# Kernel tuning notes

Measured on AMD Instinct MI355X. Metric: run time of the kernel, lower is better.

## Reference

```python
import jax, jax.numpy as jnp
import numpy as np

D_MODEL, N_HEADS = 768, 12
D_K = D_MODEL // N_HEADS
NEG = -1e9


def setup_inputs() -> dict:
    key = jax.random.key(0)
    ks = jax.random.split(key, 12)
    B, S, D = 2, 4096, D_MODEL
    s = 1.0 / np.sqrt(D)
    inp = {
        'query': jax.random.normal(ks[0], (B, S, D), jnp.float32),
        'key': jax.random.normal(ks[1], (B, S, D), jnp.float32),
        'value': jax.random.normal(ks[2], (B, S, D), jnp.float32),
        'mask': jnp.ones((B, S), jnp.int32),
        'Wq': jax.random.normal(ks[3], (D, D), jnp.float32) * s,
        'bq': jnp.zeros((D,), jnp.float32),
        'Wk': jax.random.normal(ks[4], (D, D), jnp.float32) * s,
        'bk': jnp.zeros((D,), jnp.float32),
        'Wv': jax.random.normal(ks[5], (D, D), jnp.float32) * s,
        'bv': jnp.zeros((D,), jnp.float32),
        'Wo': jax.random.normal(ks[6], (D, D), jnp.float32) * s,
        'bo': jnp.zeros((D,), jnp.float32),
    }
    return inp


def reference(query, key, value, mask, Wq, bq, Wk, bk, Wv, bv, Wo, bo):
    B, Sq, D = query.shape
    Sk = key.shape[1]
    # torch Linear: x @ W.T + b; weights stored [out, in]
    def proj(x, W, b, S):
        return (x @ W.T + b).reshape(B, S, N_HEADS, D_K).transpose(0, 2, 1, 3)
    Q = proj(query, Wq, bq, Sq)   # [B,H,Sq,Dk]
    K = proj(key, Wk, bk, Sk)
    V = proj(value, Wv, bv, Sk)
    scores = jnp.einsum('bhqd,bhkd->bhqk', Q, K) / jnp.sqrt(jnp.float32(D_K))
    # padding mask on keys: [B,1,1,Sk]
    scores = jnp.where(mask[:, None, None, :] == 0, NEG, scores)
    # causal mask (triu, diagonal=1)
    causal = jnp.triu(jnp.ones((Sq, Sk), bool), k=1)
    scores = jnp.where(causal[None, None], NEG, scores)
    attn = jax.nn.softmax(scores, axis=-1)
    out = jnp.einsum('bhqk,bhkd->bhqd', attn, V)
    out = out.transpose(0, 2, 1, 3).reshape(B, Sq, D)
    return out @ Wo.T + bo
```

## Files before the change

kernel.cpp:

```cpp
#include <hip/hip_runtime.h>
#include <hip/hip_bf16.h>

#define D_MODEL 768
#define N_HEADS 12
#define D_K     64
#define NEG_INF (-1e9f)
#define KS_PAD  72
#define VT_PAD  136
#define SCALE_Q 0.1803368801111154f
#define W_ELEMS (D_MODEL * D_MODEL)

typedef __attribute__((ext_vector_type(8))) short          bf16x8;
typedef __attribute__((ext_vector_type(4))) float          floatx4;
typedef __attribute__((ext_vector_type(4))) unsigned short ushortx4;
typedef __attribute__((ext_vector_type(2))) unsigned int   uintx2;
typedef __attribute__((ext_vector_type(4))) unsigned int   uintx4;

static __device__ __forceinline__ unsigned short f2bf(float f) {
    unsigned u = __builtin_bit_cast(unsigned, f);
    u += 0x7FFFu + ((u >> 16) & 1u);
    return (unsigned short)(u >> 16);
}

static __device__ __forceinline__ void gload_lds16(const void* g, void* l) {
    __builtin_amdgcn_global_load_lds(
        (const __attribute__((address_space(1))) void*)g,
        (__attribute__((address_space(3))) void*)l, 16, 0, 0);
}

__global__ __launch_bounds__(256) void convert_w4(
    const float* __restrict__ W0, const float* __restrict__ W1,
    const float* __restrict__ W2, const float* __restrict__ W3,
    unsigned short* __restrict__ out)
{
    const float* src[4] = {W0, W1, W2, W3};
    const float* W = src[blockIdx.y];
    unsigned short* o = out + (size_t)blockIdx.y * W_ELEMS;
    const int i = (blockIdx.x * 256 + threadIdx.x) * 4;
    float4 v = *(const float4*)(W + i);
    ushortx4 h = { f2bf(v.x), f2bf(v.y), f2bf(v.z), f2bf(v.w) };
    *(ushortx4*)(o + i) = h;
}

__global__ __launch_bounds__(256) void convert_a3(
    const float* __restrict__ A0, const float* __restrict__ A1,
    const float* __restrict__ A2,
    unsigned short* __restrict__ O0, unsigned short* __restrict__ O1,
    unsigned short* __restrict__ O2)
{
    const int z = blockIdx.y;
    const float* A = (z == 0) ? A0 : (z == 1) ? A1 : A2;
    unsigned short* O = (z == 0) ? O0 : (z == 1) ? O1 : O2;
    const int i = (blockIdx.x * 256 + threadIdx.x) * 4;
    float4 v = *(const float4*)(A + i);
    ushortx4 h = { f2bf(v.x), f2bf(v.y), f2bf(v.z), f2bf(v.w) };
    *(ushortx4*)(O + i) = h;
}

template <bool QKV>
__global__ __launch_bounds__(256) void gemm128(
    const unsigned short* __restrict__ A0, const unsigned short* __restrict__ A1,
    const unsigned short* __restrict__ A2,
    const unsigned short* __restrict__ W0, const unsigned short* __restrict__ W1,
    const unsigned short* __restrict__ W2,
    const float* __restrict__ b0, const float* __restrict__ b1,
    const float* __restrict__ b2,
    void* __restrict__ C0, void* __restrict__ C1, void* __restrict__ C2,
    int S)
{
    __shared__ __align__(16) unsigned short As[128 * 32];
    __shared__ __align__(16) unsigned short Bs[128 * 32];

    const int z = QKV ? blockIdx.z : 0;
    const unsigned short* A = (z == 0) ? A0 : (z == 1) ? A1 : A2;
    const unsigned short* W = (z == 0) ? W0 : (z == 1) ? W1 : W2;
    const float* bias       = (z == 0) ? b0 : (z == 1) ? b1 : b2;
    void* C                 = (z == 0) ? C0 : (z == 1) ? C1 : C2;
    const float scale = (QKV && z == 0) ? SCALE_Q : 1.0f;
    const int mode = QKV ? ((z == 2) ? 3 : 1) : 0;

    const int tid  = threadIdx.x;
    const int wave = tid >> 6;
    const int lane = tid & 63;
    const int quad = lane >> 4;
    const int l16  = lane & 15;
    const int m0 = blockIdx.x * 128;
    const int n0 = blockIdx.y * 128;
    const int wm = (wave & 1) * 64;
    const int wn = (wave >> 1) * 64;
    const int sr = lane >> 2;
    const int sc = (lane & 3) << 3;

    const floatx4 zero4 = {0.f, 0.f, 0.f, 0.f};
    floatx4 acc[4][4];
    #pragma unroll
    for (int i = 0; i < 4; ++i)
        #pragma unroll
        for (int j = 0; j < 4; ++j) acc[i][j] = zero4;

    for (int k0 = 0; k0 < D_MODEL; k0 += 32) {
        #pragma unroll
        for (int c = 0; c < 2; ++c) {
            const int row = wave * 32 + c * 16;
            gload_lds16(A + (size_t)(m0 + row + sr) * D_MODEL + k0 + sc,
                        As + row * 32);
            gload_lds16(W + (size_t)(n0 + row + sr) * D_MODEL + k0 + sc,
                        Bs + row * 32);
        }
        __syncthreads();

        bf16x8 af[4], bfr[4];
        #pragma unroll
        for (int i = 0; i < 4; ++i)
            af[i] = *(const bf16x8*)(As + (wm + i * 16 + l16) * 32 + quad * 8);
        #pragma unroll
        for (int j = 0; j < 4; ++j)
            bfr[j] = *(const bf16x8*)(Bs + (wn + j * 16 + l16) * 32 + quad * 8);
        #pragma unroll
        for (int i = 0; i < 4; ++i)
            #pragma unroll
            for (int j = 0; j < 4; ++j)
                acc[i][j] = __builtin_amdgcn_mfma_f32_16x16x32_bf16(
                    bfr[j], af[i], acc[i][j], 0, 0, 0);
        __syncthreads();
    }

    #pragma unroll
    for (int i = 0; i < 4; ++i) {
        const int m = m0 + wm + i * 16 + l16;
        #pragma unroll
        for (int j = 0; j < 4; ++j) {
            const int nb = n0 + wn + j * 16 + quad * 4;
            const float4 bv = *(const float4*)(bias + nb);
            float v0 = (acc[i][j][0] + bv.x) * scale;
            float v1 = (acc[i][j][1] + bv.y) * scale;
            float v2 = (acc[i][j][2] + bv.z) * scale;
            float v3 = (acc[i][j][3] + bv.w) * scale;
            if (mode == 0) {
                float4 o = {v0, v1, v2, v3};
                *(float4*)((float*)C + (size_t)m * D_MODEL + nb) = o;
            } else if (mode == 1) {
                ushortx4 o = {f2bf(v0), f2bf(v1), f2bf(v2), f2bf(v3)};
                *(ushortx4*)((unsigned short*)C + (size_t)m * D_MODEL + nb) = o;
            } else {
                const int bb = m / S, s = m - bb * S;
                const int hh = nb >> 6, d = nb & 63;
                unsigned short* base = (unsigned short*)C +
                    ((size_t)(bb * N_HEADS + hh) * D_K + d) * S + s;
                base[0]         = f2bf(v0);
                base[(size_t)S]     = f2bf(v1);
                base[(size_t)S * 2] = f2bf(v2);
                base[(size_t)S * 3] = f2bf(v3);
            }
        }
    }
}

__global__ __launch_bounds__(256) void flash_attn(
    const unsigned short* __restrict__ Qp,
    const unsigned short* __restrict__ Kp,
    const unsigned short* __restrict__ VpT,
    const int* __restrict__ mask,
    unsigned short* __restrict__ O,
    int S)
{
    __shared__ __align__(16) unsigned short Ks [128 * KS_PAD];
    __shared__ __align__(16) unsigned short Vts[64 * VT_PAD];
    __shared__ __align__(16) float mskf[128];

    const int L  = blockIdx.x;
    const int bh = L % 24;
    const int p  = L / 24;
    const int h  = bh % 12;
    const int b  = bh / 12;
    const int nqt = S >> 6;
    const int tid  = threadIdx.x;
    const int wave = tid >> 6;
    const int lane = tid & 63;
    const int quad = lane >> 4;
    const int l16  = lane & 15;

    const unsigned short* Kbase = Kp  + (size_t)(b * S) * D_MODEL + h * D_K;
    const unsigned short* Vbase = VpT + (size_t)(b * N_HEADS + h) * D_K * S;

    const floatx4 zero4 = {0.f, 0.f, 0.f, 0.f};
    const short one_bf = (short)0x3F80;
    const bf16x8 ones = {one_bf, one_bf, one_bf, one_bf,
                         one_bf, one_bf, one_bf, one_bf};

    #pragma unroll
    for (int sel = 0; sel < 2; ++sel) {
        const int qt = sel ? (nqt - 1 - p) : p;
        const int q0 = qt * 64;
        const int qbase = q0 + wave * 16;
        const int qabs = qbase + l16;

        const size_t rowQ = (size_t)(b * S + qbase + l16) * D_MODEL + h * D_K;
        const bf16x8 qf0 = *(const bf16x8*)(Qp + rowQ + quad * 8);
        const bf16x8 qf1 = *(const bf16x8*)(Qp + rowQ + 32 + quad * 8);

        floatx4 acc2[4];
        floatx4 acc_l = zero4;
        #pragma unroll
        for (int dt = 0; dt < 4; ++dt) acc2[dt] = zero4;

        const int ni = (qt >> 1) + 1;
        for (int kt = 0; kt < ni; ++kt) {
            const int k0 = kt * 128;
            #pragma unroll
            for (int g = tid; g < 1024; g += 256) {
                const int krow = g >> 3, kc = (g & 7) << 3;
                *(bf16x8*)(Ks + krow * KS_PAD + kc) =
                    *(const bf16x8*)(Kbase + (size_t)(k0 + krow) * D_MODEL + kc);
                const int vrow = g >> 4, vc = (g & 15) << 3;
                *(bf16x8*)(Vts + vrow * VT_PAD + vc) =
                    *(const bf16x8*)(Vbase + (size_t)vrow * S + k0 + vc);
            }
            if (tid < 128)
                mskf[tid] = (mask[b * S + k0 + tid] == 0) ? NEG_INF : 0.f;
            __syncthreads();

            floatx4 s[8];
            #pragma unroll
            for (int nt = 0; nt < 8; ++nt) {
                floatx4 c = *(const floatx4*)(mskf + nt * 16 + quad * 4);
                bf16x8 kf0 = *(const bf16x8*)(Ks + (nt * 16 + l16) * KS_PAD + quad * 8);
                bf16x8 kf1 = *(const bf16x8*)(Ks + (nt * 16 + l16) * KS_PAD + 32 + quad * 8);
                c = __builtin_amdgcn_mfma_f32_16x16x32_bf16(kf0, qf0, c, 0, 0, 0);
                c = __builtin_amdgcn_mfma_f32_16x16x32_bf16(kf1, qf1, c, 0, 0, 0);
                s[nt] = c;
            }

            if (kt == ni - 1) {
                #pragma unroll
                for (int nt = 0; nt < 8; ++nt) {
                    const int kb = k0 + nt * 16 + quad * 4;
                    #pragma unroll
                    for (int r = 0; r < 4; ++r)
                        if (kb + r > qabs) s[nt][r] = NEG_INF;
                }
            }

            unsigned pk0[8], pk1[8];
            #pragma unroll
            for (int nt = 0; nt < 8; ++nt) {
                const float e0 = __builtin_exp2f(s[nt][0]);
                const float e1 = __builtin_exp2f(s[nt][1]);
                const float e2 = __builtin_exp2f(s[nt][2]);
                const float e3 = __builtin_exp2f(s[nt][3]);
                pk0[nt] = __builtin_amdgcn_perm(__builtin_bit_cast(unsigned, e1),
                                                __builtin_bit_cast(unsigned, e0), 0x07060302u);
                pk1[nt] = __builtin_amdgcn_perm(__builtin_bit_cast(unsigned, e3),
                                                __builtin_bit_cast(unsigned, e2), 0x07060302u);
            }

            #pragma unroll
            for (int kh = 0; kh < 4; ++kh) {
                uintx2 a32 = __builtin_amdgcn_permlane32_swap(
                    pk0[2 * kh], pk0[2 * kh + 1], false, false);
                uintx2 b32 = __builtin_amdgcn_permlane32_swap(
                    pk1[2 * kh], pk1[2 * kh + 1], false, false);
                uintx2 a16 = __builtin_amdgcn_permlane16_swap(
                    a32[0], a32[1], false, false);
                uintx2 b16 = __builtin_amdgcn_permlane16_swap(
                    b32[0], b32[1], false, false);
                const uintx4 pw = {a16[0], b16[0], a16[1], b16[1]};
                const bf16x8 pf = __builtin_bit_cast(bf16x8, pw);
                #pragma unroll
                for (int dt = 0; dt < 4; ++dt) {
                    bf16x8 vf = *(const bf16x8*)(Vts + (dt * 16 + l16) * VT_PAD + kh * 32 + quad * 8);
                    acc2[dt] = __builtin_amdgcn_mfma_f32_16x16x32_bf16(pf, vf, acc2[dt], 0, 0, 0);
                }
                acc_l = __builtin_amdgcn_mfma_f32_16x16x32_bf16(pf, ones, acc_l, 0, 0, 0);
            }
            __syncthreads();
        }

        #pragma unroll
        for (int r = 0; r < 4; ++r) {
            const float inv = 1.f / acc_l[r];
            const int gq = qbase + quad * 4 + r;
            const size_t base = (size_t)(b * S + gq) * D_MODEL + h * D_K;
            #pragma unroll
            for (int dt = 0; dt < 4; ++dt)
                O[base + dt * 16 + l16] = f2bf(acc2[dt][r] * inv);
        }
        __syncthreads();
    }
}

extern "C" void kernel_launch(void* const* d_in, const int* in_sizes, int n_in,
                              void* d_out, int out_size, void* d_ws, size_t ws_size,
                              hipStream_t stream) {
    const float* query = (const float*)d_in[0];
    const float* key   = (const float*)d_in[1];
    const float* value = (const float*)d_in[2];
    const int*   mask  = (const int*)d_in[3];
    const float* Wq = (const float*)d_in[4];
    const float* bq = (const float*)d_in[5];
    const float* Wk = (const float*)d_in[6];
    const float* bk = (const float*)d_in[7];
    const float* Wv = (const float*)d_in[8];
    const float* bv = (const float*)d_in[9];
    const float* Wo = (const float*)d_in[10];
    const float* bo = (const float*)d_in[11];

    const int B  = 2;
    const int BS = in_sizes[3];
    const int S  = BS / B;
    const int M  = BS;

    unsigned short* Qp  = (unsigned short*)d_ws;
    unsigned short* Kp  = Qp  + (size_t)M * D_MODEL;
    unsigned short* VpT = Kp  + (size_t)M * D_MODEL;
    unsigned short* Obf = VpT + (size_t)M * D_MODEL;
    unsigned short* Wbf = Obf + (size_t)M * D_MODEL;
    unsigned short* Wqb = Wbf;
    unsigned short* Wkb = Wbf + (size_t)W_ELEMS;
    unsigned short* Wvb = Wbf + (size_t)W_ELEMS * 2;
    unsigned short* Wob = Wbf + (size_t)W_ELEMS * 3;
    unsigned short* ka = (unsigned short*)d_out;
    unsigned short* va = ka + (size_t)M * D_MODEL;

    dim3 blk(256);
    convert_w4<<<dim3(W_ELEMS / 1024, 4), blk, 0, stream>>>(Wq, Wk, Wv, Wo, Wbf);
    convert_a3<<<dim3((M * D_MODEL) / 1024, 3), blk, 0, stream>>>(
        query, key, value, Obf, ka, va);

    gemm128<true><<<dim3(M / 128, D_MODEL / 128, 3), blk, 0, stream>>>(
        Obf, ka, va, Wqb, Wkb, Wvb, bq, bk, bv, Qp, Kp, VpT, S);

    flash_attn<<<768, blk, 0, stream>>>(Qp, Kp, VpT, mask, Obf, S);

    gemm128<false><<<dim3(M / 128, D_MODEL / 128, 1), blk, 0, stream>>>(
        Obf, Obf, Obf, Wob, Wob, Wob, bo, bo, bo,
        d_out, d_out, d_out, S);
}
```

Baseline: 314.3 us.

## One query tile per block, heaviest-first, with XOR-swizzled unpadded LDS and direct mask loads

The attention kernel now assigns a single 64-row query tile to each block, launched heaviest-first (descending qt), instead of pairing a light and a heavy tile per block across 768 blocks. The grid doubles to 24*(S/64) blocks. LDS padding is replaced by an XOR swizzle on K and V^T rows, which reduces shared memory per block. Mask values are now read straight from global memory into the score accumulator init rather than staged in LDS, and __launch_bounds__ adds a 5-blocks-per-CU occupancy hint. Together these aim to improve load balance and occupancy, at the cost of more blocks and repeated global mask reads.

```diff
diff --git a/kernel.cpp b/kernel.cpp
--- a/kernel.cpp
+++ b/kernel.cpp
@@ -5,8 +5,6 @@
 #define N_HEADS 12
 #define D_K     64
 #define NEG_INF (-1e9f)
-#define KS_PAD  72
-#define VT_PAD  136
 #define SCALE_Q 0.1803368801111154f
 #define W_ELEMS (D_MODEL * D_MODEL)
 
@@ -156,7 +154,7 @@
     }
 }
 
-__global__ __launch_bounds__(256) void flash_attn(
+__global__ __launch_bounds__(256, 5) void flash_attn(
     const unsigned short* __restrict__ Qp,
     const unsigned short* __restrict__ Kp,
     const unsigned short* __restrict__ VpT,
@@ -164,128 +162,131 @@
     unsigned short* __restrict__ O,
     int S)
 {
-    __shared__ __align__(16) unsigned short Ks [128 * KS_PAD];
-    __shared__ __align__(16) unsigned short Vts[64 * VT_PAD];
-    __shared__ __align__(16) float mskf[128];
-
-    const int L  = blockIdx.x;
-    const int bh = L % 24;
-    const int p  = L / 24;
-    const int h  = bh % 12;
-    const int b  = bh / 12;
+    __shared__ __align__(16) unsigned short Ks [128 * 64];
+    __shared__ __align__(16) unsigned short Vts[64 * 128];
+
+    const int L   = blockIdx.x;
+    const int bh  = L % 24;
+    const int idx = L / 24;
+    const int h   = bh % 12;
+    const int b   = bh / 12;
     const int nqt = S >> 6;
+    const int qt  = nqt - 1 - idx;
     const int tid  = threadIdx.x;
     const int wave = tid >> 6;
     const int lane = tid & 63;
     const int quad = lane >> 4;
     const int l16  = lane & 15;
+    const int kxor = (l16 & 7) << 3;
 
     const unsigned short* Kbase = Kp  + (size_t)(b * S) * D_MODEL + h * D_K;
     const unsigned short* Vbase = VpT + (size_t)(b * N_HEADS + h) * D_K * S;
+    const int* mbase = mask + b * S;
 
     const floatx4 zero4 = {0.f, 0.f, 0.f, 0.f};
     const short one_bf = (short)0x3F80;
     const bf16x8 ones = {one_bf, one_bf, one_bf, one_bf,
                          one_bf, one_bf, one_bf, one_bf};
 
+    const int q0 = qt * 64;
+    const int qbase = q0 + wave * 16;
+    const int qabs = qbase + l16;
+
+    const size_t rowQ = (size_t)(b * S + qbase + l16) * D_MODEL + h * D_K;
+    const bf16x8 qf0 = *(const bf16x8*)(Qp + rowQ + quad * 8);
+    const bf16x8 qf1 = *(const bf16x8*)(Qp + rowQ + 32 + quad * 8);
+
+    floatx4 acc2[4];
+    floatx4 acc_l = zero4;
     #pragma unroll
-    for (int sel = 0; sel < 2; ++sel) {
-        const int qt = sel ? (nqt - 1 - p) : p;
-        const int q0 = qt * 64;
-        const int qbase = q0 + wave * 16;
-        const int qabs = qbase + l16;
-
-        const size_t rowQ = (size_t)(b * S + qbase + l16) * D_MODEL + h * D_K;
-        const bf16x8 qf0 = *(const bf16x8*)(Qp + rowQ + quad * 8);
-        const bf16x8 qf1 = *(const bf16x8*)(Qp + rowQ + 32 + quad * 8);
-
-        floatx4 acc2[4];
-        floatx4 acc_l = zero4;
-        #pragma unroll
-        for (int dt = 0; dt < 4; ++dt) acc2[dt] = zero4;
-
-        const int ni = (qt >> 1) + 1;
-        for (int kt = 0; kt < ni; ++kt) {
-            const int k0 = kt * 128;
-            #pragma unroll
-            for (int g = tid; g < 1024; g += 256) {
-                const int krow = g >> 3, kc = (g & 7) << 3;
-                *(bf16x8*)(Ks + krow * KS_PAD + kc) =
-                    *(const bf16x8*)(Kbase + (size_t)(k0 + krow) * D_MODEL + kc);
-                const int vrow = g >> 4, vc = (g & 15) << 3;
-                *(bf16x8*)(Vts + vrow * VT_PAD + vc) =
-                    *(const bf16x8*)(Vbase + (size_t)vrow * S + k0 + vc);
-            }
-            if (tid < 128)
-                mskf[tid] = (mask[b * S + k0 + tid] == 0) ? NEG_INF : 0.f;
-            __syncthreads();
-
-            floatx4 s[8];
+    for (int dt = 0; dt < 4; ++dt) acc2[dt] = zero4;
+
+    const int ni = (qt >> 1) + 1;
+    for (int kt = 0; kt < ni; ++kt) {
+        const int k0 = kt * 128;
+        #pragma unroll
+        for (int g = tid; g < 1024; g += 256) {
+            const int krow = g >> 3, kc = (g & 7) << 3;
+            *(bf16x8*)(Ks + krow * 64 + (kc ^ ((krow & 7) << 3))) =
+                *(const bf16x8*)(Kbase + (size_t)(k0 + krow) * D_MODEL + kc);
+            const int vrow = g >> 4, vc = (g & 15) << 3;
+            *(bf16x8*)(Vts + vrow * 128 + (vc ^ ((vrow & 7) << 3))) =
+                *(const bf16x8*)(Vbase + (size_t)vrow * S + k0 + vc);
+        }
+        __syncthreads();
+
+        floatx4 s[8];
+        #pragma unroll
+        for (int nt = 0; nt < 8; ++nt) {
+            const int4 mk = *(const int4*)(mbase + k0 + nt * 16 + quad * 4);
+            floatx4 c;
+            c[0] = (mk.x == 0) ? NEG_INF : 0.f;
+            c[1] = (mk.y == 0) ? NEG_INF : 0.f;
+            c[2] = (mk.z == 0) ? NEG_INF : 0.f;
+            c[3] = (mk.w == 0) ? NEG_INF : 0.f;
+            const int krow = nt * 16 + l16;
+            bf16x8 kf0 = *(const bf16x8*)(Ks + krow * 64 + ((quad * 8) ^ kxor));
+            bf16x8 kf1 = *(const bf16x8*)(Ks + krow * 64 + ((32 + quad * 8) ^ kxor));
+            c = __builtin_amdgcn_mfma_f32_16x16x32_bf16(kf0, qf0, c, 0, 0, 0);
+            c = __builtin_amdgcn_mfma_f32_16x16x32_bf16(kf1, qf1, c, 0, 0, 0);
+            s[nt] = c;
+        }
+
+        if (kt == ni - 1) {
             #pragma unroll
             for (int nt = 0; nt < 8; ++nt) {
-                floatx4 c = *(const floatx4*)(mskf + nt * 16 + quad * 4);
-                bf16x8 kf0 = *(const bf16x8*)(Ks + (nt * 16 + l16) * KS_PAD + quad * 8);
-                bf16x8 kf1 = *(const bf16x8*)(Ks + (nt * 16 + l16) * KS_PAD + 32 + quad * 8);
-                c = __builtin_amdgcn_mfma_f32_16x16x32_bf16(kf0, qf0, c, 0, 0, 0);
-                c = __builtin_amdgcn_mfma_f32_16x16x32_bf16(kf1, qf1, c, 0, 0, 0);
-                s[nt] = c;
+                const int kb = k0 + nt * 16 + quad * 4;
+                #pragma unroll
+                for (int r = 0; r < 4; ++r)
+                    if (kb + r > qabs) s[nt][r] = NEG_INF;
             }
-
-            if (kt == ni - 1) {
-                #pragma unroll
-                for (int nt = 0; nt < 8; ++nt) {
-                    const int kb = k0 + nt * 16 + quad * 4;
-                    #pragma unroll
-                    for (int r = 0; r < 4; ++r)
-                        if (kb + r > qabs) s[nt][r] = NEG_INF;
-                }
+        }
+
+        unsigned pk0[8], pk1[8];
+        #pragma unroll
+        for (int nt = 0; nt < 8; ++nt) {
+            const float e0 = __builtin_exp2f(s[nt][0]);
+            const float e1 = __builtin_exp2f(s[nt][1]);
+            const float e2 = __builtin_exp2f(s[nt][2]);
+            const float e3 = __builtin_exp2f(s[nt][3]);
+            pk0[nt] = __builtin_amdgcn_perm(__builtin_bit_cast(unsigned, e1),
+                                            __builtin_bit_cast(unsigned, e0), 0x07060302u);
+            pk1[nt] = __builtin_amdgcn_perm(__builtin_bit_cast(unsigned, e3),
+                                            __builtin_bit_cast(unsigned, e2), 0x07060302u);
+        }
+
+        #pragma unroll
+        for (int kh = 0; kh < 4; ++kh) {
+            uintx2 a32 = __builtin_amdgcn_permlane32_swap(
+                pk0[2 * kh], pk0[2 * kh + 1], false, false);
+            uintx2 b32 = __builtin_amdgcn_permlane32_swap(
+                pk1[2 * kh], pk1[2 * kh + 1], false, false);
+            uintx2 a16 = __builtin_amdgcn_permlane16_swap(
+                a32[0], a32[1], false, false);
+            uintx2 b16 = __builtin_amdgcn_permlane16_swap(
+                b32[0], b32[1], false, false);
+            const uintx4 pw = {a16[0], b16[0], a16[1], b16[1]};
+            const bf16x8 pf = __builtin_bit_cast(bf16x8, pw);
+            #pragma unroll
+            for (int dt = 0; dt < 4; ++dt) {
+                const int vrow = dt * 16 + l16;
+                bf16x8 vf = *(const bf16x8*)(
+                    Vts + vrow * 128 + ((kh * 32 + quad * 8) ^ kxor));
+                acc2[dt] = __builtin_amdgcn_mfma_f32_16x16x32_bf16(pf, vf, acc2[dt], 0, 0, 0);
             }
-
-            unsigned pk0[8], pk1[8];
-            #pragma unroll
-            for (int nt = 0; nt < 8; ++nt) {
-                const float e0 = __builtin_exp2f(s[nt][0]);
-                const float e1 = __builtin_exp2f(s[nt][1]);
-                const float e2 = __builtin_exp2f(s[nt][2]);
-                const float e3 = __builtin_exp2f(s[nt][3]);
-                pk0[nt] = __builtin_amdgcn_perm(__builtin_bit_cast(unsigned, e1),
-                                                __builtin_bit_cast(unsigned, e0), 0x07060302u);
-                pk1[nt] = __builtin_amdgcn_perm(__builtin_bit_cast(unsigned, e3),
-                                                __builtin_bit_cast(unsigned, e2), 0x07060302u);
-            }
-
-            #pragma unroll
-            for (int kh = 0; kh < 4; ++kh) {
-                uintx2 a32 = __builtin_amdgcn_permlane32_swap(
-                    pk0[2 * kh], pk0[2 * kh + 1], false, false);
-                uintx2 b32 = __builtin_amdgcn_permlane32_swap(
-                    pk1[2 * kh], pk1[2 * kh + 1], false, false);
-                uintx2 a16 = __builtin_amdgcn_permlane16_swap(
-                    a32[0], a32[1], false, false);
-                uintx2 b16 = __builtin_amdgcn_permlane16_swap(
-                    b32[0], b32[1], false, false);
-                const uintx4 pw = {a16[0], b16[0], a16[1], b16[1]};
-                const bf16x8 pf = __builtin_bit_cast(bf16x8, pw);
-                #pragma unroll
-                for (int dt = 0; dt < 4; ++dt) {
-                    bf16x8 vf = *(const bf16x8*)(Vts + (dt * 16 + l16) * VT_PAD + kh * 32 + quad * 8);
-                    acc2[dt] = __builtin_amdgcn_mfma_f32_16x16x32_bf16(pf, vf, acc2[dt], 0, 0, 0);
-                }
-                acc_l = __builtin_amdgcn_mfma_f32_16x16x32_bf16(pf, ones, acc_l, 0, 0, 0);
-            }
-            __syncthreads();
-        }
-
-        #pragma unroll
-        for (int r = 0; r < 4; ++r) {
-            const float inv = 1.f / acc_l[r];
-            const int gq = qbase + quad * 4 + r;
-            const size_t base = (size_t)(b * S + gq) * D_MODEL + h * D_K;
-            #pragma unroll
-            for (int dt = 0; dt < 4; ++dt)
-                O[base + dt * 16 + l16] = f2bf(acc2[dt][r] * inv);
+            acc_l = __builtin_amdgcn_mfma_f32_16x16x32_bf16(pf, ones, acc_l, 0, 0, 0);
         }
         __syncthreads();
+    }
+
+    #pragma unroll
+    for (int r = 0; r < 4; ++r) {
+        const float inv = 1.f / acc_l[r];
+        const int gq = qbase + quad * 4 + r;
+        const size_t base = (size_t)(b * S + gq) * D_MODEL + h * D_K;
+        #pragma unroll
+        for (int dt = 0; dt < 4; ++dt)
+            O[base + dt * 16 + l16] = f2bf(acc2[dt][r] * inv);
     }
 }
 
@@ -330,7 +331,7 @@
     gemm128<true><<<dim3(M / 128, D_MODEL / 128, 3), blk, 0, stream>>>(
         Obf, ka, va, Wqb, Wkb, Wvb, bq, bk, bv, Qp, Kp, VpT, S);
 
-    flash_attn<<<768, blk, 0, stream>>>(Qp, Kp, VpT, mask, Obf, S);
+    flash_attn<<<dim3(24 * (S / 64)), blk, 0, stream>>>(Qp, Kp, VpT, mask, Obf, S);
 
     gemm128<false><<<dim3(M / 128, D_MODEL / 128, 1), blk, 0, stream>>>(
         Obf, Obf, Obf, Wob, Wob, Wob, bo, bo, bo,
```

Result: slower. 419.8 us (+33.6%).

## Double-buffer K tiles via register prefetch and read V directly from global

Applied to the files above, without the earlier changes.

The flash attention loop now prefetches the next K tile and its mask into registers while computing the current tile, then writes them into a second LDS buffer, which removes one barrier per iteration. The V tile is no longer staged in shared memory: each wave reads its V fragments straight from the transposed global V array. This is meant to hide global-load latency and lower LDS use, but it makes the four waves each fetch V redundantly from global or L2 memory.

```diff
diff --git a/kernel.cpp b/kernel.cpp
--- a/kernel.cpp
+++ b/kernel.cpp
@@ -6,7 +6,6 @@
 #define D_K     64
 #define NEG_INF (-1e9f)
 #define KS_PAD  72
-#define VT_PAD  136
 #define SCALE_Q 0.1803368801111154f
 #define W_ELEMS (D_MODEL * D_MODEL)
 
@@ -164,9 +163,8 @@
     unsigned short* __restrict__ O,
     int S)
 {
-    __shared__ __align__(16) unsigned short Ks [128 * KS_PAD];
-    __shared__ __align__(16) unsigned short Vts[64 * VT_PAD];
-    __shared__ __align__(16) float mskf[128];
+    __shared__ __align__(16) unsigned short Ks[2][128 * KS_PAD];
+    __shared__ __align__(16) float mskf[2][128];
 
     const int L  = blockIdx.x;
     const int bh = L % 24;
@@ -182,11 +180,15 @@
 
     const unsigned short* Kbase = Kp  + (size_t)(b * S) * D_MODEL + h * D_K;
     const unsigned short* Vbase = VpT + (size_t)(b * N_HEADS + h) * D_K * S;
+    const int* mbase = mask + b * S;
 
     const floatx4 zero4 = {0.f, 0.f, 0.f, 0.f};
     const short one_bf = (short)0x3F80;
     const bf16x8 ones = {one_bf, one_bf, one_bf, one_bf,
                          one_bf, one_bf, one_bf, one_bf};
+
+    const int srow = tid >> 3;
+    const int scol = (tid & 7) << 3;
 
     #pragma unroll
     for (int sel = 0; sel < 2; ++sel) {
@@ -205,27 +207,42 @@
         for (int dt = 0; dt < 4; ++dt) acc2[dt] = zero4;
 
         const int ni = (qt >> 1) + 1;
+
+        bf16x8 kr[4];
+        float mr = 0.f;
+
+        #pragma unroll
+        for (int c = 0; c < 4; ++c)
+            kr[c] = *(const bf16x8*)(
+                Kbase + (size_t)(c * 32 + srow) * D_MODEL + scol);
+        if (tid < 128) mr = (mbase[tid] == 0) ? NEG_INF : 0.f;
+        #pragma unroll
+        for (int c = 0; c < 4; ++c)
+            *(bf16x8*)(&Ks[0][(c * 32 + srow) * KS_PAD + scol]) = kr[c];
+        if (tid < 128) mskf[0][tid] = mr;
+        __syncthreads();
+
         for (int kt = 0; kt < ni; ++kt) {
             const int k0 = kt * 128;
-            #pragma unroll
-            for (int g = tid; g < 1024; g += 256) {
-                const int krow = g >> 3, kc = (g & 7) << 3;
-                *(bf16x8*)(Ks + krow * KS_PAD + kc) =
-                    *(const bf16x8*)(Kbase + (size_t)(k0 + krow) * D_MODEL + kc);
-                const int vrow = g >> 4, vc = (g & 15) << 3;
-                *(bf16x8*)(Vts + vrow * VT_PAD + vc) =
-                    *(const bf16x8*)(Vbase + (size_t)vrow * S + k0 + vc);
-            }
-            if (tid < 128)
-                mskf[tid] = (mask[b * S + k0 + tid] == 0) ? NEG_INF : 0.f;
-            __syncthreads();
+            const int cur = kt & 1;
+            const bool pre = (kt + 1 < ni);
+
+            if (pre) {
+                const int kn = k0 + 128;
+                #pragma unroll
+                for (int c = 0; c < 4; ++c)
+                    kr[c] = *(const bf16x8*)(
+                        Kbase + (size_t)(kn + c * 32 + srow) * D_MODEL + scol);
+                if (tid < 128) mr = (mbase[kn + tid] == 0) ? NEG_INF : 0.f;
+            }
 
             floatx4 s[8];
             #pragma unroll
             for (int nt = 0; nt < 8; ++nt) {
-                floatx4 c = *(const floatx4*)(mskf + nt * 16 + quad * 4);
-                bf16x8 kf0 = *(const bf16x8*)(Ks + (nt * 16 + l16) * KS_PAD + quad * 8);
-                bf16x8 kf1 = *(const bf16x8*)(Ks + (nt * 16 + l16) * KS_PAD + 32 + quad * 8);
+                floatx4 c = *(const floatx4*)(&mskf[cur][nt * 16 + quad * 4]);
+                const unsigned short* kro = &Ks[cur][(nt * 16 + l16) * KS_PAD];
+                bf16x8 kf0 = *(const bf16x8*)(kro + quad * 8);
+                bf16x8 kf1 = *(const bf16x8*)(kro + 32 + quad * 8);
                 c = __builtin_amdgcn_mfma_f32_16x16x32_bf16(kf0, qf0, c, 0, 0, 0);
                 c = __builtin_amdgcn_mfma_f32_16x16x32_bf16(kf1, qf1, c, 0, 0, 0);
                 s[nt] = c;
@@ -254,6 +271,7 @@
                                                 __builtin_bit_cast(unsigned, e2), 0x07060302u);
             }
 
+            const unsigned short* Vk = Vbase + k0;
             #pragma unroll
             for (int kh = 0; kh < 4; ++kh) {
                 uintx2 a32 = __builtin_amdgcn_permlane32_swap(
@@ -268,10 +286,18 @@
                 const bf16x8 pf = __builtin_bit_cast(bf16x8, pw);
                 #pragma unroll
                 for (int dt = 0; dt < 4; ++dt) {
-                    bf16x8 vf = *(const bf16x8*)(Vts + (dt * 16 + l16) * VT_PAD + kh * 32 + quad * 8);
+                    bf16x8 vf = *(const bf16x8*)(
+                        Vk + (size_t)(dt * 16 + l16) * S + kh * 32 + quad * 8);
                     acc2[dt] = __builtin_amdgcn_mfma_f32_16x16x32_bf16(pf, vf, acc2[dt], 0, 0, 0);
                 }
                 acc_l = __builtin_amdgcn_mfma_f32_16x16x32_bf16(pf, ones, acc_l, 0, 0, 0);
+            }
+
+            if (pre) {
+                #pragma unroll
+                for (int c = 0; c < 4; ++c)
+                    *(bf16x8*)(&Ks[cur ^ 1][(c * 32 + srow) * KS_PAD + scol]) = kr[c];
+                if (tid < 128) mskf[cur ^ 1][tid] = mr;
             }
             __syncthreads();
         }
```

Result: slower. 502.8 us (+60.0%).

## Load K/V tiles with direct global-to-LDS copies and XOR-swizzled layout

Applied to the files above, without the earlier changes.

Replaces register-staged global→LDS copies of the K and V tiles with global_load_lds direct transfers. The padded LDS rows are swapped for unpadded rows with an XOR swizzle on the column index, so reads stay free of bank conflicts. This removes the VGPR round trip and the separate LDS store instructions in the tile-load loop. The swizzle indexing has to match the lane-to-address mapping of the direct loads exactly, which adds some complexity.

```diff
diff --git a/kernel.cpp b/kernel.cpp
--- a/kernel.cpp
+++ b/kernel.cpp
@@ -5,8 +5,6 @@
 #define N_HEADS 12
 #define D_K     64
 #define NEG_INF (-1e9f)
-#define KS_PAD  72
-#define VT_PAD  136
 #define SCALE_Q 0.1803368801111154f
 #define W_ELEMS (D_MODEL * D_MODEL)
 
@@ -164,8 +162,8 @@
     unsigned short* __restrict__ O,
     int S)
 {
-    __shared__ __align__(16) unsigned short Ks [128 * KS_PAD];
-    __shared__ __align__(16) unsigned short Vts[64 * VT_PAD];
+    __shared__ __align__(16) unsigned short Ks [128 * 64];
+    __shared__ __align__(16) unsigned short Vts[64 * 128];
     __shared__ __align__(16) float mskf[128];
 
     const int L  = blockIdx.x;
@@ -179,9 +177,17 @@
     const int lane = tid & 63;
     const int quad = lane >> 4;
     const int l16  = lane & 15;
+    const int sx   = (l16 & 7) << 3;
 
     const unsigned short* Kbase = Kp  + (size_t)(b * S) * D_MODEL + h * D_K;
     const unsigned short* Vbase = VpT + (size_t)(b * N_HEADS + h) * D_K * S;
+    const int* mbase = mask + b * S;
+
+    const int kgrow = wave * 32 + (lane >> 3);
+    const int kgcol = ((lane & 7) ^ (lane >> 3)) << 3;
+    const int vgrow = wave * 16 + (lane >> 4);
+    const int vgc_e = ((lane & 15) ^ (lane >> 4)) << 3;
+    const int vgc_o = ((lane & 15) ^ (4 + (lane >> 4))) << 3;
 
     const floatx4 zero4 = {0.f, 0.f, 0.f, 0.f};
     const short one_bf = (short)0x3F80;
@@ -208,24 +214,26 @@
         for (int kt = 0; kt < ni; ++kt) {
             const int k0 = kt * 128;
             #pragma unroll
-            for (int g = tid; g < 1024; g += 256) {
-                const int krow = g >> 3, kc = (g & 7) << 3;
-                *(bf16x8*)(Ks + krow * KS_PAD + kc) =
-                    *(const bf16x8*)(Kbase + (size_t)(k0 + krow) * D_MODEL + kc);
-                const int vrow = g >> 4, vc = (g & 15) << 3;
-                *(bf16x8*)(Vts + vrow * VT_PAD + vc) =
-                    *(const bf16x8*)(Vbase + (size_t)vrow * S + k0 + vc);
+            for (int c = 0; c < 4; ++c) {
+                gload_lds16(
+                    Kbase + (size_t)(k0 + kgrow + c * 8) * D_MODEL + kgcol,
+                    (char*)Ks + (wave * 4 + c) * 1024);
+                const int vg = (c & 1) ? vgc_o : vgc_e;
+                gload_lds16(
+                    Vbase + (size_t)(vgrow + c * 4) * S + k0 + vg,
+                    (char*)Vts + (wave * 4 + c) * 1024);
             }
             if (tid < 128)
-                mskf[tid] = (mask[b * S + k0 + tid] == 0) ? NEG_INF : 0.f;
+                mskf[tid] = (mbase[k0 + tid] == 0) ? NEG_INF : 0.f;
             __syncthreads();
 
             floatx4 s[8];
             #pragma unroll
             for (int nt = 0; nt < 8; ++nt) {
                 floatx4 c = *(const floatx4*)(mskf + nt * 16 + quad * 4);
-                bf16x8 kf0 = *(const bf16x8*)(Ks + (nt * 16 + l16) * KS_PAD + quad * 8);
-                bf16x8 kf1 = *(const bf16x8*)(Ks + (nt * 16 + l16) * KS_PAD + 32 + quad * 8);
+                const unsigned short* kro = Ks + (nt * 16 + l16) * 64;
+                bf16x8 kf0 = *(const bf16x8*)(kro + ((quad * 8) ^ sx));
+                bf16x8 kf1 = *(const bf16x8*)(kro + ((32 + quad * 8) ^ sx));
                 c = __builtin_amdgcn_mfma_f32_16x16x32_bf16(kf0, qf0, c, 0, 0, 0);
                 c = __builtin_amdgcn_mfma_f32_16x16x32_bf16(kf1, qf1, c, 0, 0, 0);
                 s[nt] = c;
@@ -268,7 +276,8 @@
                 const bf16x8 pf = __builtin_bit_cast(bf16x8, pw);
                 #pragma unroll
                 for (int dt = 0; dt < 4; ++dt) {
-                    bf16x8 vf = *(const bf16x8*)(Vts + (dt * 16 + l16) * VT_PAD + kh * 32 + quad * 8);
+                    const unsigned short* vro = Vts + (dt * 16 + l16) * 128;
+                    bf16x8 vf = *(const bf16x8*)(vro + ((kh * 32 + quad * 8) ^ sx));
                     acc2[dt] = __builtin_amdgcn_mfma_f32_16x16x32_bf16(pf, vf, acc2[dt], 0, 0, 0);
                 }
                 acc_l = __builtin_amdgcn_mfma_f32_16x16x32_bf16(pf, ones, acc_l, 0, 0, 0);
```

Measured after the change: 306.2 us. 1.03x faster.
